# Optimization experiments

Measured on AMD Instinct MI355X. Metric: run time of the kernel, lower is better.

Reference implementation:

```python
import jax, jax.numpy as jnp
import numpy as np

NEG_INF = -1e30


def setup_inputs() -> dict:
    key = jax.random.key(0)
    kx, km, kq, kk, kv, ko = jax.random.split(key, 6)
    B, D, L = 2, 1024, 2048
    H, DK = 16, 64
    x = jax.random.normal(kx, (B, D, L), dtype=jnp.float32)
    mask = (jax.random.uniform(km, (B, L)) < 0.9).astype(jnp.float32)
    # per-head projection weights, stacked: (H, D, DK); output proj (D, H*DK)==(D, D)
    sq = 1.0 / np.sqrt(D)
    Wq = jax.random.normal(kq, (H, D, DK), dtype=jnp.float32) * sq
    Wk = jax.random.normal(kk, (H, D, DK), dtype=jnp.float32) * sq
    Wv = jax.random.normal(kv, (H, D, DK), dtype=jnp.float32) * sq
    Wo = jax.random.normal(ko, (D, H * DK), dtype=jnp.float32) * sq
    return {"x": x, "mask": mask, "Wq": Wq, "Wk": Wk, "Wv": Wv, "Wo": Wo}


def reference(x, mask, Wq, Wk, Wv, Wo):
    # x: (B, D, L); original transposes to (B, L, D)
    B, D, L = x.shape
    H, _, DK = Wq.shape
    xt = jnp.transpose(x, (0, 2, 1))  # (B, L, D)
    q = jnp.einsum('bld,hdk->bhlk', xt, Wq)
    k = jnp.einsum('bld,hdk->bhlk', xt, Wk)
    v = jnp.einsum('bld,hdk->bhlk', xt, Wv)
    scores = jnp.einsum('bhlk,bhmk->bhlm', q, k) * (1.0 / np.sqrt(DK))
    # masked log-softmax over keys (hmask), squad-style: mask*logit + (1-mask)*-1e30
    hmask = mask[:, None, None, :]  # (B,1,1,Lk)
    masked = hmask * scores + (1.0 - hmask) * NEG_INF
    logp = jax.nn.log_softmax(masked, axis=-1)
    # second softmax over the log-probs, then multiplicative vmask on query dim
    p = jax.nn.softmax(logp, axis=-1) * mask[:, None, :, None]
    heads = jnp.einsum('bhlm,bhmk->bhlk', p, v)  # (B,H,L,DK)
    head = jnp.transpose(heads, (0, 2, 1, 3)).reshape(B, L, H * DK)
    out = jnp.einsum('ble,de->bld', head, Wo)  # matmul(head, Wo) with Wo (D, H*DK)... 
    # NOTE: torch.matmul(head, Wo) treats Wo as (H*DK_in, D_out) only if square; here
    # Wo is (D, H*DK) with D == H*DK, and torch contracts head's last dim with Wo's FIRST dim:
    out = head @ Wo  # (B, L, H*DK) @ (D, H*DK) requires D==H*DK; contracts dim 0 of Wo
    return jnp.transpose(out, (0, 2, 1))  # (B, D, L)


if __name__ == "__main__":
    print(reference(**setup_inputs()).shape)
```

## Files before the change

### kernel.cpp

```cpp
#include <hip/hip_runtime.h>
#include <hip/hip_bf16.h>

typedef unsigned short u16;
typedef unsigned int u32;
typedef unsigned long long u64;
typedef short s8v __attribute__((ext_vector_type(8)));
typedef short s4v __attribute__((ext_vector_type(4)));
typedef __bf16 bfv8 __attribute__((ext_vector_type(8)));
typedef float f4 __attribute__((ext_vector_type(4)));

static constexpr int B = 2, D = 1024, L = 2048, H = 16, DK = 64, E = 1024;
static constexpr float QSCALE = 0.125f * 1.44269504088896340736f;
static constexpr float SMB = -16.0f;
static constexpr float MASKB = -12000.0f;

#define DEV __device__ __forceinline__

DEV u16 f2bf(float f) {
  unsigned int u = __float_as_uint(f);
  u += 0x7FFFu + ((u >> 16) & 1u);
  return (u16)(u >> 16);
}
DEV float fexp2(float x) { return __builtin_amdgcn_exp2f(x); }
DEV u32 pkbf(float a, float b) {
  __hip_bfloat162 h = __float22bfloat162_rn(float2{a, b});
  u32 r;
  __builtin_memcpy(&r, &h, 4);
  return r;
}

DEV f4 mfma16(s4v a, s4v b, f4 c) {
  return __builtin_amdgcn_mfma_f32_16x16x16bf16_1k(a, b, c, 0, 0, 0);
}

#define GLD_LDS16(gp, lp)                                                     \
  __builtin_amdgcn_global_load_lds(                                           \
      (const __attribute__((address_space(1))) void*)(gp),                    \
      (__attribute__((address_space(3))) void*)(lp), 16, 0, 0)

__global__ __launch_bounds__(256) void k_prep(
    const float* __restrict__ x, const float* __restrict__ Wq,
    const float* __restrict__ Wk, const float* __restrict__ Wv,
    const float* __restrict__ Wo, u16* __restrict__ xt, u16* __restrict__ Wt,
    u16* __restrict__ WoT) {
  __shared__ u16 t[64][67];
  const int tid = threadIdx.x;
  const int g = blockIdx.x;
  const float* src;
  u16* dst;
  int sld, dld;
  if (g < 1024) {
    const int b = g >> 9, dt = (g >> 5) & 15, lt = g & 31;
    src = x + ((size_t)b * D + dt * 64) * L + lt * 64;
    sld = L;
    dst = xt + ((size_t)b * L + lt * 64) * D + dt * 64;
    dld = D;
  } else if (g < 1792) {
    const int u = g - 1024;
    const int w = u >> 8, h = (u >> 4) & 15, dt = u & 15;
    const float* Ws = (w == 0) ? Wq : ((w == 1) ? Wk : Wv);
    src = Ws + ((size_t)h * D + dt * 64) * DK;
    sld = DK;
    dst = Wt + ((size_t)(w * H + h) * DK) * D + dt * 64;
    dld = D;
  } else {
    const int v = g - 1792;
    const int et = v >> 4, dt = v & 15;
    src = Wo + ((size_t)et * 64) * D + dt * 64;
    sld = D;
    dst = WoT + ((size_t)dt * 64) * E + et * 64;
    dld = E;
  }
  const int r = tid >> 2, c16 = (tid & 3) * 16;
#pragma unroll
  for (int j = 0; j < 16; j += 4) {
    const f4 v4 = *(const f4*)(src + (size_t)r * sld + c16 + j);
    t[r][c16 + j]     = f2bf(v4[0]);
    t[r][c16 + j + 1] = f2bf(v4[1]);
    t[r][c16 + j + 2] = f2bf(v4[2]);
    t[r][c16 + j + 3] = f2bf(v4[3]);
  }
  __syncthreads();
  s8v o0, o1;
#pragma unroll
  for (int i = 0; i < 8; ++i) {
    o0[i] = (short)t[c16 + i][r];
    o1[i] = (short)t[c16 + 8 + i][r];
  }
  *(s8v*)(dst + (size_t)r * dld + c16)     = o0;
  *(s8v*)(dst + (size_t)r * dld + c16 + 8) = o1;
}

template <int AR>
DEV void gemm_tile(const u16* __restrict__ A, const u16* __restrict__ Bt,
                   int arow0, int brow0, u16* As, u16* Bs,
                   f4 (&acc)[AR / 32][4]) {
  const int tid = threadIdx.x;
  const int wid = tid >> 6, lane = tid & 63;
  const int q = lane >> 4, ln = lane & 15;
  const int wr = wid >> 1, wc = wid & 1;
  const int lrow = lane >> 2;
  const int lcg = (lane & 3) ^ ((lane >> 3) & 3);
  const int scA = (q ^ ((ln >> 1) & 3)) * 8;
  constexpr int MT = AR / 32;

  for (int k0 = 0; k0 < 1024; k0 += 32) {
    __syncthreads();
#pragma unroll
    for (int j = 0; j < AR / 64; ++j) {
      const int rb = wid * (AR / 4) + j * 16;
      GLD_LDS16(A + (size_t)(arow0 + rb + lrow) * 1024 + k0 + lcg * 8,
                As + rb * 32);
    }
#pragma unroll
    for (int j = 0; j < 2; ++j) {
      const int rb = wid * 32 + j * 16;
      GLD_LDS16(Bt + (size_t)(brow0 + rb + lrow) * 1024 + k0 + lcg * 8,
                Bs + rb * 32);
    }
    __syncthreads();
    bfv8 af[MT], bf[4];
#pragma unroll
    for (int mt = 0; mt < MT; ++mt)
      af[mt] = *(const bfv8*)(As + (wr * (AR / 2) + mt * 16 + ln) * 32 + scA);
#pragma unroll
    for (int nt = 0; nt < 4; ++nt)
      bf[nt] = *(const bfv8*)(Bs + (wc * 64 + nt * 16 + ln) * 32 + scA);
#pragma unroll
    for (int mt = 0; mt < MT; ++mt)
#pragma unroll
      for (int nt = 0; nt < 4; ++nt)
        acc[mt][nt] = __builtin_amdgcn_mfma_f32_16x16x32_bf16(
            af[mt], bf[nt], acc[mt][nt], 0, 0, 0);
  }
}

__global__ __launch_bounds__(256, 3) void k_qkvg(
    const u16* __restrict__ xt, const u16* __restrict__ Wt,
    u16* __restrict__ Q, u16* __restrict__ K, u16* __restrict__ Vt) {
  __shared__ u16 As[128 * 32];
  __shared__ u16 Bs[128 * 32];
  const int bm = blockIdx.x, bn = blockIdx.y;
  f4 acc[4][4];
#pragma unroll
  for (int mt = 0; mt < 4; ++mt)
#pragma unroll
    for (int nt = 0; nt < 4; ++nt) acc[mt][nt] = (f4){0.f, 0.f, 0.f, 0.f};
  gemm_tile<128>(xt, Wt, bm * 128, bn * 128, As, Bs, acc);

  const int tid = threadIdx.x, wid = tid >> 6, lane = tid & 63;
  const int q = lane >> 4, ln = lane & 15;
  const int wr = wid >> 1, wc = wid & 1;
  const int h2 = bn * 2 + wc;
  const int wsel = h2 >> 4, h = h2 & 15;
  const int b = bm >> 4;
  const int lbase = (bm & 15) * 128 + wr * 64;
  if (wsel == 0) {
    u16* dst = Q + (size_t)(b * H + h) * L * DK;
#pragma unroll
    for (int mt = 0; mt < 4; ++mt)
#pragma unroll
      for (int nt = 0; nt < 4; ++nt)
#pragma unroll
        for (int r = 0; r < 4; ++r)
          dst[(size_t)(lbase + mt * 16 + q * 4 + r) * DK + nt * 16 + ln] =
              f2bf(acc[mt][nt][r] * QSCALE);
  } else if (wsel == 1) {
    u16* dst = K + (size_t)(b * H + h) * L * DK;
#pragma unroll
    for (int mt = 0; mt < 4; ++mt)
#pragma unroll
      for (int nt = 0; nt < 4; ++nt)
#pragma unroll
        for (int r = 0; r < 4; ++r)
          dst[(size_t)(lbase + mt * 16 + q * 4 + r) * DK + nt * 16 + ln] =
              f2bf(acc[mt][nt][r]);
  } else {
    u16* dst = Vt + (size_t)(b * H + h) * DK * L;
#pragma unroll
    for (int mt = 0; mt < 4; ++mt)
#pragma unroll
      for (int nt = 0; nt < 4; ++nt) {
        const u64 pk = (u64)pkbf(acc[mt][nt][0], acc[mt][nt][1]) |
                       ((u64)pkbf(acc[mt][nt][2], acc[mt][nt][3]) << 32);
        *(u64*)(dst + (size_t)(nt * 16 + ln) * L + lbase + mt * 16 + q * 4) =
            pk;
      }
  }
}

__global__ __launch_bounds__(256, 4) void k_attn(
    const u16* __restrict__ Q, const u16* __restrict__ K,
    const u16* __restrict__ Vt, const float* __restrict__ mask,
    u16* __restrict__ Hd) {
  __shared__ u16 kt[2][64 * 64];
  __shared__ u16 vt[2][64 * 64];
  __shared__ __align__(16) float mb[L];
  const int h = blockIdx.x, lt = blockIdx.y, b = blockIdx.z;
  const int tid = threadIdx.x;
  const int w = tid >> 6, lane = tid & 63, q = lane >> 4, ln = lane & 15;
  for (int i = tid; i < L; i += 256)
    mb[i] = (mask[(size_t)b * L + i] != 0.0f) ? SMB : MASKB;

  const int bh = b * H + h;
  const u16* Qp = Q + (size_t)bh * L * DK;
  const u16* Kp = K + (size_t)bh * L * DK;
  const u16* Vp = Vt + (size_t)bh * DK * L;
  const int lq = lt * 64 + w * 16;

  const bfv8 qf0 = *(const bfv8*)(Qp + (size_t)(lq + ln) * DK + q * 8);
  const bfv8 qf1 = *(const bfv8*)(Qp + (size_t)(lq + ln) * DK + 32 + q * 8);

  const int lrow = lane >> 3;
  const int lc = (lane & 7) ^ lrow;
  const int fr0 = w * 16 + lrow, fr1 = fr0 + 8;
  const int c0 = (q ^ (ln & 7)) * 8;
  const int c1 = ((q + 4) ^ (ln & 7)) * 8;

  auto stage = [&](int m0, int bufi) {
    GLD_LDS16(Kp + (size_t)(m0 + fr0) * DK + lc * 8, &kt[bufi][(w * 16) * 64]);
    GLD_LDS16(Kp + (size_t)(m0 + fr1) * DK + lc * 8,
              &kt[bufi][(w * 16 + 8) * 64]);
    GLD_LDS16(Vp + (size_t)fr0 * L + m0 + lc * 8, &vt[bufi][(w * 16) * 64]);
    GLD_LDS16(Vp + (size_t)fr1 * L + m0 + lc * 8, &vt[bufi][(w * 16 + 8) * 64]);
  };

  f4 ot[4];
#pragma unroll
  for (int i = 0; i < 4; ++i) ot[i] = (f4){0.f, 0.f, 0.f, 0.f};
  float lp = 0.f;

  stage(0, 0);
  for (int it = 0; it < L / 64; ++it) {
    const int m0 = it * 64;
    __syncthreads();
    if (it + 1 < L / 64) stage(m0 + 64, (it + 1) & 1);
    const u16* ktc = &kt[it & 1][0];
    const u16* vtc = &vt[it & 1][0];

    f4 s[4];
#pragma unroll
    for (int nt = 0; nt < 4; ++nt) {
      const int krow = nt * 16 + ln;
      const bfv8 kf0 = *(const bfv8*)(ktc + krow * 64 + c0);
      const bfv8 kf1 = *(const bfv8*)(ktc + krow * 64 + c1);
      f4 a = *(const f4*)(mb + m0 + nt * 16 + q * 4);
      a = __builtin_amdgcn_mfma_f32_16x16x32_bf16(kf0, qf0, a, 0, 0, 0);
      a = __builtin_amdgcn_mfma_f32_16x16x32_bf16(kf1, qf1, a, 0, 0, 0);
      s[nt] = a;
    }
    s4v pb[4];
#pragma unroll
    for (int nt = 0; nt < 4; ++nt) {
      const float p0 = fexp2(s[nt][0]);
      const float p1 = fexp2(s[nt][1]);
      const float p2 = fexp2(s[nt][2]);
      const float p3 = fexp2(s[nt][3]);
      lp += (p0 + p1) + (p2 + p3);
      const u64 pk = (u64)pkbf(p0, p1) | ((u64)pkbf(p2, p3) << 32);
      pb[nt] = __builtin_bit_cast(s4v, pk);
    }
#pragma unroll
    for (int dt = 0; dt < 4; ++dt) {
      const int vrow = dt * 16 + ln;
      const int vbase = vrow * 64 + (q & 1) * 4;
      const int rx = vrow & 7;
      f4 a = ot[dt];
#pragma unroll
      for (int kc = 0; kc < 4; ++kc) {
        const s4v av =
            *(const s4v*)(vtc + vbase + (((kc * 2 + (q >> 1)) ^ rx) * 8));
        a = mfma16(av, pb[kc], a);
      }
      ot[dt] = a;
    }
  }
  lp += __shfl_xor(lp, 16);
  lp += __shfl_xor(lp, 32);
  const float linv = (mb[lq + ln] > -100.0f) ? (1.0f / lp) : 0.0f;
#pragma unroll
  for (int dt = 0; dt < 4; ++dt) {
    const u64 pk =
        (u64)pkbf(ot[dt][0] * linv, ot[dt][1] * linv) |
        ((u64)pkbf(ot[dt][2] * linv, ot[dt][3] * linv) << 32);
    *(u64*)(Hd + (size_t)(b * L + lq + ln) * E + h * DK + dt * 16 + q * 4) = pk;
  }
}

__global__ __launch_bounds__(256, 2) void k_projg(const u16* __restrict__ WoT,
                                                  const u16* __restrict__ Hd,
                                                  float* __restrict__ out) {
  __shared__ u16 As[64 * 32];
  __shared__ u16 Bs[128 * 32];
  const int bm = blockIdx.x, bn = blockIdx.y;
  f4 acc[2][4];
#pragma unroll
  for (int mt = 0; mt < 2; ++mt)
#pragma unroll
    for (int nt = 0; nt < 4; ++nt) acc[mt][nt] = (f4){0.f, 0.f, 0.f, 0.f};
  gemm_tile<64>(WoT, Hd, bm * 64, bn * 128, As, Bs, acc);

  const int tid = threadIdx.x, wid = tid >> 6, lane = tid & 63;
  const int q = lane >> 4, ln = lane & 15;
  const int wr = wid >> 1, wc = wid & 1;
#pragma unroll
  for (int mt = 0; mt < 2; ++mt)
#pragma unroll
    for (int nt = 0; nt < 4; ++nt)
#pragma unroll
      for (int r = 0; r < 4; ++r) {
        const int d = bm * 64 + wr * 32 + mt * 16 + q * 4 + r;
        const int n = bn * 128 + wc * 64 + nt * 16 + ln;
        const int bb = n >> 11, l = n & 2047;
        out[((size_t)(bb * D + d)) * L + l] = acc[mt][nt][r];
      }
}

extern "C" void kernel_launch(void* const* d_in, const int* in_sizes, int n_in,
                              void* d_out, int out_size, void* d_ws,
                              size_t ws_size, hipStream_t stream) {
  const float* x    = (const float*)d_in[0];
  const float* mask = (const float*)d_in[1];
  const float* Wq   = (const float*)d_in[2];
  const float* Wk   = (const float*)d_in[3];
  const float* Wv   = (const float*)d_in[4];
  const float* Wo   = (const float*)d_in[5];
  u16* ws = (u16*)d_ws;
  u16* Qws  = ws;
  u16* Kws  = ws + 4194304;
  u16* Vtws = ws + 8388608;
  u16* WoTw = ws + 12582912;
  u16* Wtws = ws + 13631488;
  u16* xtws = ws + 16777216;
  u16* Hdws = ws + 16777216;

  k_prep<<<2048, 256, 0, stream>>>(x, Wq, Wk, Wv, Wo, xtws, Wtws, WoTw);
  k_qkvg<<<dim3(32, 24), 256, 0, stream>>>(xtws, Wtws, Qws, Kws, Vtws);
  k_attn<<<dim3(16, 32, 2), 256, 0, stream>>>(Qws, Kws, Vtws, mask, Hdws);
  k_projg<<<dim3(16, 32), 256, 0, stream>>>(WoTw, Hdws, (float*)d_out);
}
```

Measured before the change: 189.6 us.

## Process two query tiles per wave in attention to reuse K/V LDS loads

Each wave in the attention kernel now handles 32 query rows (two 16-row MFMA tiles) instead of 16, so a block covers 128 queries and the grid halves along the sequence. Each K fragment, mask-bias vector and V fragment read from LDS now feeds two MFMAs instead of one. This halves total K/V global staging and LDS reads per query. In exchange, register pressure roughly doubles for accumulators and scores, launch bounds drop to 2 blocks per CU, and there are half as many blocks (512) to fill the GPU.

```diff
diff --git a/kernel.cpp b/kernel.cpp
--- a/kernel.cpp
+++ b/kernel.cpp
@@ -189,7 +189,7 @@
   }
 }
 
-__global__ __launch_bounds__(256, 4) void k_attn(
+__global__ __launch_bounds__(256, 2) void k_attn(
     const u16* __restrict__ Q, const u16* __restrict__ K,
     const u16* __restrict__ Vt, const float* __restrict__ mask,
     u16* __restrict__ Hd) {
@@ -206,10 +206,15 @@
   const u16* Qp = Q + (size_t)bh * L * DK;
   const u16* Kp = K + (size_t)bh * L * DK;
   const u16* Vp = Vt + (size_t)bh * DK * L;
-  const int lq = lt * 64 + w * 16;
-
-  const bfv8 qf0 = *(const bfv8*)(Qp + (size_t)(lq + ln) * DK + q * 8);
-  const bfv8 qf1 = *(const bfv8*)(Qp + (size_t)(lq + ln) * DK + 32 + q * 8);
+  const int lq = lt * 128 + w * 32;
+
+  bfv8 qf[2][2];
+#pragma unroll
+  for (int mt = 0; mt < 2; ++mt) {
+    qf[mt][0] = *(const bfv8*)(Qp + (size_t)(lq + mt * 16 + ln) * DK + q * 8);
+    qf[mt][1] =
+        *(const bfv8*)(Qp + (size_t)(lq + mt * 16 + ln) * DK + 32 + q * 8);
+  }
 
   const int lrow = lane >> 3;
   const int lc = (lane & 7) ^ lrow;
@@ -225,10 +230,12 @@
     GLD_LDS16(Vp + (size_t)fr1 * L + m0 + lc * 8, &vt[bufi][(w * 16 + 8) * 64]);
   };
 
-  f4 ot[4];
-#pragma unroll
-  for (int i = 0; i < 4; ++i) ot[i] = (f4){0.f, 0.f, 0.f, 0.f};
-  float lp = 0.f;
+  f4 ot[2][4];
+#pragma unroll
+  for (int mt = 0; mt < 2; ++mt)
+#pragma unroll
+    for (int i = 0; i < 4; ++i) ot[mt][i] = (f4){0.f, 0.f, 0.f, 0.f};
+  float lp[2] = {0.f, 0.f};
 
   stage(0, 0);
   for (int it = 0; it < L / 64; ++it) {
@@ -238,52 +245,70 @@
     const u16* ktc = &kt[it & 1][0];
     const u16* vtc = &vt[it & 1][0];
 
-    f4 s[4];
+    bfv8 kf0[4], kf1[4];
+    f4 mbv[4];
 #pragma unroll
     for (int nt = 0; nt < 4; ++nt) {
       const int krow = nt * 16 + ln;
-      const bfv8 kf0 = *(const bfv8*)(ktc + krow * 64 + c0);
-      const bfv8 kf1 = *(const bfv8*)(ktc + krow * 64 + c1);
-      f4 a = *(const f4*)(mb + m0 + nt * 16 + q * 4);
-      a = __builtin_amdgcn_mfma_f32_16x16x32_bf16(kf0, qf0, a, 0, 0, 0);
-      a = __builtin_amdgcn_mfma_f32_16x16x32_bf16(kf1, qf1, a, 0, 0, 0);
-      s[nt] = a;
-    }
-    s4v pb[4];
-#pragma unroll
-    for (int nt = 0; nt < 4; ++nt) {
-      const float p0 = fexp2(s[nt][0]);
-      const float p1 = fexp2(s[nt][1]);
-      const float p2 = fexp2(s[nt][2]);
-      const float p3 = fexp2(s[nt][3]);
-      lp += (p0 + p1) + (p2 + p3);
-      const u64 pk = (u64)pkbf(p0, p1) | ((u64)pkbf(p2, p3) << 32);
-      pb[nt] = __builtin_bit_cast(s4v, pk);
-    }
+      kf0[nt] = *(const bfv8*)(ktc + krow * 64 + c0);
+      kf1[nt] = *(const bfv8*)(ktc + krow * 64 + c1);
+      mbv[nt] = *(const f4*)(mb + m0 + nt * 16 + q * 4);
+    }
+    f4 s[2][4];
+#pragma unroll
+    for (int nt = 0; nt < 4; ++nt)
+#pragma unroll
+      for (int mt = 0; mt < 2; ++mt) {
+        f4 a = mbv[nt];
+        a = __builtin_amdgcn_mfma_f32_16x16x32_bf16(kf0[nt], qf[mt][0], a, 0,
+                                                    0, 0);
+        a = __builtin_amdgcn_mfma_f32_16x16x32_bf16(kf1[nt], qf[mt][1], a, 0,
+                                                    0, 0);
+        s[mt][nt] = a;
+      }
+    s4v pb[2][4];
+#pragma unroll
+    for (int mt = 0; mt < 2; ++mt)
+#pragma unroll
+      for (int nt = 0; nt < 4; ++nt) {
+        const float p0 = fexp2(s[mt][nt][0]);
+        const float p1 = fexp2(s[mt][nt][1]);
+        const float p2 = fexp2(s[mt][nt][2]);
+        const float p3 = fexp2(s[mt][nt][3]);
+        lp[mt] += (p0 + p1) + (p2 + p3);
+        const u64 pk = (u64)pkbf(p0, p1) | ((u64)pkbf(p2, p3) << 32);
+        pb[mt][nt] = __builtin_bit_cast(s4v, pk);
+      }
 #pragma unroll
     for (int dt = 0; dt < 4; ++dt) {
       const int vrow = dt * 16 + ln;
       const int vbase = vrow * 64 + (q & 1) * 4;
       const int rx = vrow & 7;
-      f4 a = ot[dt];
-#pragma unroll
-      for (int kc = 0; kc < 4; ++kc) {
-        const s4v av =
-            *(const s4v*)(vtc + vbase + (((kc * 2 + (q >> 1)) ^ rx) * 8));
-        a = mfma16(av, pb[kc], a);
-      }
-      ot[dt] = a;
-    }
-  }
-  lp += __shfl_xor(lp, 16);
-  lp += __shfl_xor(lp, 32);
-  const float linv = (mb[lq + ln] > -100.0f) ? (1.0f / lp) : 0.0f;
-#pragma unroll
-  for (int dt = 0; dt < 4; ++dt) {
-    const u64 pk =
-        (u64)pkbf(ot[dt][0] * linv, ot[dt][1] * linv) |
-        ((u64)pkbf(ot[dt][2] * linv, ot[dt][3] * linv) << 32);
-    *(u64*)(Hd + (size_t)(b * L + lq + ln) * E + h * DK + dt * 16 + q * 4) = pk;
+      s4v av[4];
+#pragma unroll
+      for (int kc = 0; kc < 4; ++kc)
+        av[kc] = *(const s4v*)(vtc + vbase + (((kc * 2 + (q >> 1)) ^ rx) * 8));
+#pragma unroll
+      for (int kc = 0; kc < 4; ++kc)
+#pragma unroll
+        for (int mt = 0; mt < 2; ++mt)
+          ot[mt][dt] = mfma16(av[kc], pb[mt][kc], ot[mt][dt]);
+    }
+  }
+#pragma unroll
+  for (int mt = 0; mt < 2; ++mt) {
+    lp[mt] += __shfl_xor(lp[mt], 16);
+    lp[mt] += __shfl_xor(lp[mt], 32);
+    const float linv =
+        (mb[lq + mt * 16 + ln] > -100.0f) ? (1.0f / lp[mt]) : 0.0f;
+#pragma unroll
+    for (int dt = 0; dt < 4; ++dt) {
+      const u64 pk =
+          (u64)pkbf(ot[mt][dt][0] * linv, ot[mt][dt][1] * linv) |
+          ((u64)pkbf(ot[mt][dt][2] * linv, ot[mt][dt][3] * linv) << 32);
+      *(u64*)(Hd + (size_t)(b * L + lq + mt * 16 + ln) * E + h * DK + dt * 16 +
+              q * 4) = pk;
+    }
   }
 }
 
@@ -336,6 +361,6 @@
 
   k_prep<<<2048, 256, 0, stream>>>(x, Wq, Wk, Wv, Wo, xtws, Wtws, WoTw);
   k_qkvg<<<dim3(32, 24), 256, 0, stream>>>(xtws, Wtws, Qws, Kws, Vtws);
-  k_attn<<<dim3(16, 32, 2), 256, 0, stream>>>(Qws, Kws, Vtws, mask, Hdws);
+  k_attn<<<dim3(16, 16, 2), 256, 0, stream>>>(Qws, Kws, Vtws, mask, Hdws);
   k_projg<<<dim3(16, 32), 256, 0, stream>>>(WoTw, Hdws, (float*)d_out);
 }
```

After: 188.2 us. Within noise of the previous version (-0.7%).
